# Kernel tuning notes

Hardware: AMD Instinct MI355X
Metric: run time of the kernel (lower is better)

The kernel has to match this reference:

```python
import jax, jax.numpy as jnp
import numpy as np

E = 192; Q = 48; H = 3; HD = Q // H  # per-branch embed 48, 3 heads of 16
CONV_CH = 4; K = 15; PAD = K // 2


def layer_norm(x, g, b, eps=1e-6):
    m = jnp.mean(x, axis=-1, keepdims=True)
    v = jnp.mean((x - m) ** 2, axis=-1, keepdims=True)
    return (x - m) * jax.lax.rsqrt(v + eps) * g + b


def mha(x, w_in, b_in, w_o, b_o):
    # x: [B,S,48]; torch nn.MultiheadAttention math (dropout=eval/identity)
    B, S, _ = x.shape
    qkv = x @ w_in.T + b_in                      # [B,S,144]
    q, k, v = jnp.split(qkv, 3, axis=-1)
    q = q.reshape(B, S, H, HD)
    k = k.reshape(B, S, H, HD)
    v = v.reshape(B, S, H, HD)
    scores = jnp.einsum('bqhd,bkhd->bhqk', q, k) / jnp.sqrt(jnp.float32(HD))
    attn = jax.nn.softmax(scores, axis=-1)
    out = jnp.einsum('bhqk,bkhd->bqhd', attn, v).reshape(B, S, Q)
    return out @ w_o.T + b_o


def light_conv(x96, conv_w):
    # x96: [B,S,96] -> view(-1, 4, 96), depthwise conv1d (k=15, pad=7), view back
    B, S, W = x96.shape
    r = x96.reshape(-1, CONV_CH, W)              # [B*S/... wait: B*S*96/(4*96)=B*S/4? No: reshape(-1,4,96) => [B*S, ...]
    y = jax.lax.conv_general_dilated(
        r, conv_w, window_strides=(1,), padding=[(PAD, PAD)],
        dimension_numbers=('NCH', 'OIH', 'NCH'), feature_group_count=CONV_CH)
    return y.reshape(B, S, W)


def setup_inputs() -> dict:
    key = jax.random.key(0)
    ks = jax.random.split(key, 16)
    sc = 0.05
    d = {
        'x': jax.random.normal(ks[0], (128, 512, E), dtype=jnp.float32),
        'ln1_g': jnp.ones((E,), jnp.float32), 'ln1_b': jnp.zeros((E,), jnp.float32),
        'acc_wqkv': jax.random.normal(ks[1], (3 * Q, Q), jnp.float32) * sc,
        'acc_bqkv': jnp.zeros((3 * Q,), jnp.float32),
        'acc_wo': jax.random.normal(ks[2], (Q, Q), jnp.float32) * sc,
        'acc_bo': jnp.zeros((Q,), jnp.float32),
        'gyro_wqkv': jax.random.normal(ks[3], (3 * Q, Q), jnp.float32) * sc,
        'gyro_bqkv': jnp.zeros((3 * Q,), jnp.float32),
        'gyro_wo': jax.random.normal(ks[4], (Q, Q), jnp.float32) * sc,
        'gyro_bo': jnp.zeros((Q,), jnp.float32),
        'conv_w': jax.random.normal(ks[5], (CONV_CH, 1, K), jnp.float32) * sc,
        'ln2_g': jnp.ones((E,), jnp.float32), 'ln2_b': jnp.zeros((E,), jnp.float32),
        'w1': jax.random.normal(ks[6], (2 * E, E), jnp.float32) * sc,
        'b1': jnp.zeros((2 * E,), jnp.float32),
        'w2': jax.random.normal(ks[7], (E, 2 * E), jnp.float32) * sc,
        'b2': jnp.zeros((E,), jnp.float32),
    }
    return d


def reference(x, ln1_g, ln1_b, acc_wqkv, acc_bqkv, acc_wo, acc_bo,
              gyro_wqkv, gyro_bqkv, gyro_wo, gyro_bo, conv_w,
              ln2_g, ln2_b, w1, b1, w2, b2):
    xn = layer_norm(x, ln1_g, ln1_b)
    x_conv = light_conv(xn[:, :, 48:144], conv_w)
    x_acc = mha(xn[:, :, 0:48], acc_wqkv, acc_bqkv, acc_wo, acc_bo)
    x_gyro = mha(xn[:, :, 96:144], gyro_wqkv, gyro_bqkv, gyro_wo, gyro_bo)
    xcat = jnp.concatenate([x_acc, x_conv, x_gyro], axis=2)
    x1 = xcat + x
    tt = layer_norm(x1, ln2_g, ln2_b)
    tt = jax.nn.relu(tt @ w1.T + b1)
    tt = jax.nn.relu(tt @ w2.T + b2)
    return x1 + tt
```

## Files before the change

### kernel.cpp

```cpp
#include <hip/hip_runtime.h>
#include <stdint.h>

typedef unsigned short u16;
typedef short bf16x8 __attribute__((ext_vector_type(8)));
typedef float f32x4 __attribute__((ext_vector_type(4)));
typedef float f32x16 __attribute__((ext_vector_type(16)));
typedef uint32_t u32x4 __attribute__((ext_vector_type(4)));

#define NB   128
#define SEQ  512
#define EMB  192
#define NTOK (NB * SEQ)
#define F1DIM 384
#define ATTW 192
#define VTP  520
#define KTS  24
#define XnS  200
#define H1S  392

__device__ __forceinline__ float bf2f(u16 u) {
  union { uint32_t u; float f; } v; v.u = ((uint32_t)u) << 16; return v.f;
}
__device__ __forceinline__ u16 f2bf(float f) {
  union { float f; uint32_t u; } v; v.f = f;
  uint32_t r = v.u + 0x7fffu + ((v.u >> 16) & 1u);
  return (u16)(r >> 16);
}
__device__ __forceinline__ uint32_t pack2bf(float a, float b) {
  return (uint32_t)f2bf(a) | ((uint32_t)f2bf(b) << 16);
}

__global__ __launch_bounds__(256) void pack_kernel(const float* __restrict__ w1,
    const float* __restrict__ w2, const float* __restrict__ wqa,
    const float* __restrict__ wqg, const float* __restrict__ woa,
    const float* __restrict__ wog, u16* __restrict__ w1b, u16* __restrict__ w2b,
    u16* __restrict__ wqp, u16* __restrict__ wop) {
  int idx = (int)blockIdx.x * 256 + (int)threadIdx.x;
  if (idx < 73728) {
    w1b[idx] = f2bf(w1[idx]);
  } else if (idx < 147456) {
    w2b[idx - 73728] = f2bf(w2[idx - 73728]);
  } else if (idx < 165888) {
    int i = idx - 147456;
    int row = i >> 6, k = i & 63;
    float v = 0.0f;
    if (k < 48) v = (row < 144) ? wqa[row * 48 + k] : wqg[(row - 144) * 48 + k];
    wqp[i] = f2bf(v);
  } else if (idx < 172032) {
    int i = idx - 165888;
    int row = i >> 6, k = i & 63;
    float v = 0.0f;
    if (k < 48) v = (row < 48) ? woa[row * 48 + k] : wog[(row - 48) * 48 + k];
    wop[i] = f2bf(v);
  }
}

__global__ __launch_bounds__(256) void ln1_qkv_conv_kernel(
    const float* __restrict__ x, const float* __restrict__ g,
    const float* __restrict__ b, const u16* __restrict__ wq,
    const float* __restrict__ bacc, const float* __restrict__ bgyr,
    const float* __restrict__ cw, u16* __restrict__ qkv,
    u16* __restrict__ att) {
  __shared__ u16 Xn[64 * XnS];
  int bm = (int)blockIdx.x * 64;
  int tid = threadIdx.x;
  int trow = tid >> 2, part = tid & 3;
  int tok = bm + trow;
  const float* xr = x + (size_t)tok * EMB + part * 48;
  float vals[48];
#pragma unroll
  for (int j = 0; j < 48; j += 4) {
    float4 v = *(const float4*)(xr + j);
    vals[j] = v.x; vals[j + 1] = v.y; vals[j + 2] = v.z; vals[j + 3] = v.w;
  }
  float s = 0.0f, s2 = 0.0f;
#pragma unroll
  for (int j = 0; j < 48; j++) { s += vals[j]; s2 += vals[j] * vals[j]; }
  s += __shfl_xor(s, 1); s2 += __shfl_xor(s2, 1);
  s += __shfl_xor(s, 2); s2 += __shfl_xor(s2, 2);
  float mean = s * (1.0f / EMB);
  float var  = s2 * (1.0f / EMB) - mean * mean;
  float rs   = rsqrtf(var + 1e-6f);
  {
    u16* xnrow = Xn + trow * XnS + part * 48;
    const float* gp = g + part * 48;
    const float* bp = b + part * 48;
#pragma unroll
    for (int j = 0; j < 48; j += 2) {
      uint32_t w = pack2bf((vals[j] - mean) * rs * gp[j] + bp[j],
                           (vals[j + 1] - mean) * rs * gp[j + 1] + bp[j + 1]);
      *(uint32_t*)(xnrow + j) = w;
    }
  }
  __syncthreads();
  int wid = tid >> 6, lane = tid & 63;
  int l15 = lane & 15, quad = lane >> 4;
  const u16* arow_l = Xn + (wid * 16 + l15) * XnS;
  f32x4 acc[18] = {};
#pragma unroll
  for (int ks = 0; ks < 2; ks++) {
    int kk = ks * 32;
    bf16x8 af_a = *(const bf16x8*)(arow_l + kk + quad * 8);
    bf16x8 af_g = *(const bf16x8*)(arow_l + 96 + kk + quad * 8);
#pragma unroll
    for (int st = 0; st < 18; st++) {
      bf16x8 bf = *(const bf16x8*)(wq + (size_t)(st * 16 + l15) * 64 + kk + quad * 8);
      acc[st] = __builtin_amdgcn_mfma_f32_16x16x32_bf16(st < 9 ? af_a : af_g,
                                                        bf, acc[st], 0, 0, 0);
    }
  }
#pragma unroll
  for (int st = 0; st < 18; st++) {
    int col = st * 16 + l15;
    int cc = (col < 144) ? col : col - 144;
    float bias = (col < 144) ? bacc[cc] : bgyr[cc];
    float qs = (cc < 48) ? 0.36067376022f : 1.0f;
#pragma unroll
    for (int r = 0; r < 4; r++) {
      int orow = bm + wid * 16 + quad * 4 + r;
      qkv[(size_t)orow * 288 + col] = f2bf((acc[st][r] + bias) * qs);
    }
  }
  {
    int wr = trow & 3;
    float w15[15];
#pragma unroll
    for (int k = 0; k < 15; k++) w15[k] = cw[wr * 15 + k];
    float win[38];
    int base = part * 24 - 7;
#pragma unroll
    for (int i = 0; i < 38; i++) {
      int p = base + i;
      win[i] = (p >= 0 && p < 96) ? bf2f(Xn[trow * XnS + 48 + p]) : 0.0f;
    }
    const float* xres = x + (size_t)tok * EMB + 48 + part * 24;
    u16* orow = att + (size_t)tok * ATTW + 96 + part * 24;
#pragma unroll
    for (int c = 0; c < 24; c += 4) {
      float4 r4 = *(const float4*)(xres + c);
      float o[4];
#pragma unroll
      for (int u = 0; u < 4; u++) {
        float sc = 0.0f;
#pragma unroll
        for (int k = 0; k < 15; k++) sc += win[c + u + k] * w15[k];
        o[u] = sc;
      }
      *(uint32_t*)(orow + c)     = pack2bf(o[0] + r4.x, o[1] + r4.y);
      *(uint32_t*)(orow + c + 2) = pack2bf(o[2] + r4.z, o[3] + r4.w);
    }
  }
}

__global__ __launch_bounds__(256) void attn_kernel(const u16* __restrict__ qkv,
                                                   u16* __restrict__ att) {
  __shared__ u16 Kt[SEQ * KTS];
  __shared__ u16 Vt[17 * VTP];
  int bid = blockIdx.x;
  int hh  = bid % 3;
  int brb = (bid / 3) & 1;
  int b   = bid / 6;
  int tid = threadIdx.x;
  size_t tokbase = (size_t)b * SEQ;
  int qoff = brb * 144 + hh * 16;
  int koff = qoff + 48;
  int voff = qoff + 96;
  for (int r = tid; r < SEQ; r += 256) {
    const u16* src = qkv + (tokbase + r) * 288;
    *(uint4*)(Kt + r * KTS)     = *(const uint4*)(src + koff);
    *(uint4*)(Kt + r * KTS + 8) = *(const uint4*)(src + koff + 8);
    u16 tmp[16];
    *(uint4*)(tmp)     = *(const uint4*)(src + voff);
    *(uint4*)(tmp + 8) = *(const uint4*)(src + voff + 8);
#pragma unroll
    for (int j = 0; j < 16; j++) Vt[j * VTP + r] = tmp[j];
  }
  Vt[16 * VTP + tid]       = 0x3F80;
  Vt[16 * VTP + 256 + tid] = 0x3F80;
  __syncthreads();
  int wave = tid >> 6, lane = tid & 63;
  int q31 = lane & 31, h = lane >> 5;
  int dcl = (q31 < 16) ? q31 : 16;
#pragma unroll 1
  for (int qi = 0; qi < 4; qi++) {
    int qrow = (wave * 4 + qi) * 32 + q31;
    bf16x8 qfrag = *(const bf16x8*)(qkv + (tokbase + qrow) * 288 + qoff + h * 8);
    f32x16 Ot = {};
#pragma unroll 2
    for (int kt = 0; kt < 16; kt++) {
      bf16x8 kfrag = *(const bf16x8*)(Kt + (kt * 32 + q31) * KTS + h * 8);
      f32x16 zc = {};
      f32x16 S = __builtin_amdgcn_mfma_f32_32x32x16_bf16(kfrag, qfrag, zc, 0, 0, 0);
      uint32_t pk[8], swk[8];
#pragma unroll
      for (int i = 0; i < 8; i++) {
        union { float f; uint32_t u; } a0, a1;
        a0.f = exp2f(S[2 * i]);
        a1.f = exp2f(S[2 * i + 1]);
        pk[i] = __builtin_amdgcn_perm(a1.u, a0.u, 0x07060302u);
        swk[i] = (uint32_t)__shfl_xor((int)pk[i], 32);
      }
      u32x4 t1 = { h ? swk[2] : pk[0], h ? swk[3] : pk[1],
                   h ? pk[2]  : swk[0], h ? pk[3]  : swk[1] };
      u32x4 t2 = { h ? swk[6] : pk[4], h ? swk[7] : pk[5],
                   h ? pk[6]  : swk[4], h ? pk[7]  : swk[5] };
      bf16x8 pb1 = __builtin_bit_cast(bf16x8, t1);
      bf16x8 pb2 = __builtin_bit_cast(bf16x8, t2);
      bf16x8 av1 = *(const bf16x8*)(Vt + dcl * VTP + kt * 32 + h * 8);
      bf16x8 av2 = *(const bf16x8*)(Vt + dcl * VTP + kt * 32 + 16 + h * 8);
      Ot = __builtin_amdgcn_mfma_f32_32x32x16_bf16(av1, pb1, Ot, 0, 0, 0);
      Ot = __builtin_amdgcn_mfma_f32_32x32x16_bf16(av2, pb2, Ot, 0, 0, 0);
    }
    float inv = 1.0f / Ot[8];
    u16* orow = att + (tokbase + qrow) * ATTW + brb * 48 + hh * 16 + 4 * h;
    uint2 st0 = { pack2bf(Ot[0] * inv, Ot[1] * inv),
                  pack2bf(Ot[2] * inv, Ot[3] * inv) };
    uint2 st1 = { pack2bf(Ot[4] * inv, Ot[5] * inv),
                  pack2bf(Ot[6] * inv, Ot[7] * inv) };
    *(uint2*)(orow)     = st0;
    *(uint2*)(orow + 8) = st1;
  }
}

__global__ __launch_bounds__(512) void tail_kernel(
    const u16* __restrict__ att, const u16* __restrict__ wo,
    const float* __restrict__ boacc, const float* __restrict__ bogyr,
    const float* __restrict__ x, const float* __restrict__ g2,
    const float* __restrict__ b2v, const u16* __restrict__ w1b,
    const float* __restrict__ b1, const u16* __restrict__ w2b,
    const float* __restrict__ b2, float* __restrict__ out) {
  __shared__ u16 LDSB[32 * XnS + 32 * H1S];
  u16* X1b = LDSB;
  u16* Tn  = LDSB + 32 * XnS;
  u16* H1  = LDSB + 32 * XnS;
  int bm = (int)blockIdx.x * 32;
  int tid = threadIdx.x;
  int wid = tid >> 6, lane = tid & 63;
  int l15 = lane & 15, quad = lane >> 4;

  if (wid >= 6) {
    int trow = (wid - 6) * 16 + (lane >> 2), p4 = lane & 3;
    const u16* src = att + (size_t)(bm + trow) * ATTW + 96 + p4 * 24;
    u16* dst = X1b + trow * XnS + 48 + p4 * 24;
    *(uint4*)(dst)      = *(const uint4*)(src);
    *(uint4*)(dst + 8)  = *(const uint4*)(src + 8);
    *(uint4*)(dst + 16) = *(const uint4*)(src + 16);
  } else {
    int st = wid;
    int ng = (st >= 3) ? 1 : 0;
    f32x4 acc[2] = {};
    bf16x8 wf[2];
#pragma unroll
    for (int ks = 0; ks < 2; ks++)
      wf[ks] = *(const bf16x8*)(wo + (size_t)(st * 16 + l15) * 64 + ks * 32 + quad * 8);
#pragma unroll
    for (int m = 0; m < 2; m++) {
      const u16* arow = att + (size_t)(bm + m * 16 + l15) * ATTW + (ng ? 48 : 0);
#pragma unroll
      for (int ks = 0; ks < 2; ks++) {
        bf16x8 af = *(const bf16x8*)(arow + ks * 32 + quad * 8);
        acc[m] = __builtin_amdgcn_mfma_f32_16x16x32_bf16(af, wf[ks], acc[m], 0, 0, 0);
      }
    }
    int col = st * 16 + l15;
    float bias = (col < 48) ? boacc[col] : bogyr[col - 48];
    int oc = (col < 48) ? col : col + 96;
#pragma unroll
    for (int m = 0; m < 2; m++) {
#pragma unroll
      for (int r = 0; r < 4; r++) {
        int lrow = m * 16 + quad * 4 + r;
        float v = acc[m][r] + bias + x[(size_t)(bm + lrow) * EMB + oc];
        X1b[lrow * XnS + oc] = f2bf(v);
      }
    }
  }
  __syncthreads();

  {
    int trow = tid >> 4, part = tid & 15;
    const u16* xl = X1b + trow * XnS + part * 12;
    u16 raw[12];
    *(uint2*)(raw)     = *(const uint2*)(xl);
    *(uint2*)(raw + 4) = *(const uint2*)(xl + 4);
    *(uint2*)(raw + 8) = *(const uint2*)(xl + 8);
    float vals[12];
#pragma unroll
    for (int j = 0; j < 12; j++) vals[j] = bf2f(raw[j]);
    float s = 0.0f, s2 = 0.0f;
#pragma unroll
    for (int j = 0; j < 12; j++) { s += vals[j]; s2 += vals[j] * vals[j]; }
    s += __shfl_xor(s, 1); s2 += __shfl_xor(s2, 1);
    s += __shfl_xor(s, 2); s2 += __shfl_xor(s2, 2);
    s += __shfl_xor(s, 4); s2 += __shfl_xor(s2, 4);
    s += __shfl_xor(s, 8); s2 += __shfl_xor(s2, 8);
    float mean = s * (1.0f / EMB);
    float var  = s2 * (1.0f / EMB) - mean * mean;
    float rs   = rsqrtf(var + 1e-6f);
    u16* trp = Tn + trow * XnS + part * 12;
    const float* gp = g2 + part * 12;
    const float* bp = b2v + part * 12;
#pragma unroll
    for (int j = 0; j < 12; j += 2) {
      uint32_t w = pack2bf((vals[j] - mean) * rs * gp[j] + bp[j],
                           (vals[j + 1] - mean) * rs * gp[j + 1] + bp[j + 1]);
      *(uint32_t*)(trp + j) = w;
    }
  }
  __syncthreads();

  int mg = wid & 1, ng = wid >> 1;
  f32x4 acc1[6] = {};
#pragma unroll
  for (int kk = 0; kk < 192; kk += 32) {
    bf16x8 a0 = *(const bf16x8*)(Tn + (mg * 16 + l15) * XnS + kk + quad * 8);
#pragma unroll
    for (int stl = 0; stl < 6; stl++) {
      bf16x8 bf = *(const bf16x8*)(w1b + (size_t)((ng * 6 + stl) * 16 + l15) * EMB + kk + quad * 8);
      acc1[stl] = __builtin_amdgcn_mfma_f32_16x16x32_bf16(a0, bf, acc1[stl], 0, 0, 0);
    }
  }
  __syncthreads();
#pragma unroll
  for (int stl = 0; stl < 6; stl++) {
    int col = (ng * 6 + stl) * 16 + l15;
    float bias = b1[col];
#pragma unroll
    for (int r = 0; r < 4; r++) {
      float v = acc1[stl][r] + bias;
      v = v > 0.0f ? v : 0.0f;
      H1[(mg * 16 + quad * 4 + r) * H1S + col] = f2bf(v);
    }
  }
  __syncthreads();

  {
    f32x4 acc2[3] = {};
#pragma unroll
    for (int kk = 0; kk < 384; kk += 32) {
      bf16x8 a0 = *(const bf16x8*)(H1 + (mg * 16 + l15) * H1S + kk + quad * 8);
#pragma unroll
      for (int stl = 0; stl < 3; stl++) {
        bf16x8 bf = *(const bf16x8*)(w2b + (size_t)((ng * 3 + stl) * 16 + l15) * F1DIM + kk + quad * 8);
        acc2[stl] = __builtin_amdgcn_mfma_f32_16x16x32_bf16(a0, bf, acc2[stl], 0, 0, 0);
      }
    }
#pragma unroll
    for (int stl = 0; stl < 3; stl++) {
      int col = (ng * 3 + stl) * 16 + l15;
      float bias = b2[col];
#pragma unroll
      for (int r = 0; r < 4; r++) {
        int lrow = mg * 16 + quad * 4 + r;
        float v = acc2[stl][r] + bias;
        v = v > 0.0f ? v : 0.0f;
        out[(size_t)(bm + lrow) * EMB + col] = v + bf2f(X1b[lrow * XnS + col]);
      }
    }
  }
}

extern "C" void kernel_launch(void* const* d_in, const int* in_sizes, int n_in,
                              void* d_out, int out_size, void* d_ws, size_t ws_size,
                              hipStream_t stream) {
  const float* x         = (const float*)d_in[0];
  const float* ln1_g     = (const float*)d_in[1];
  const float* ln1_b     = (const float*)d_in[2];
  const float* acc_wqkv  = (const float*)d_in[3];
  const float* acc_bqkv  = (const float*)d_in[4];
  const float* acc_wo    = (const float*)d_in[5];
  const float* acc_bo    = (const float*)d_in[6];
  const float* gyro_wqkv = (const float*)d_in[7];
  const float* gyro_bqkv = (const float*)d_in[8];
  const float* gyro_wo   = (const float*)d_in[9];
  const float* gyro_bo   = (const float*)d_in[10];
  const float* conv_w    = (const float*)d_in[11];
  const float* ln2_g     = (const float*)d_in[12];
  const float* ln2_b     = (const float*)d_in[13];
  const float* w1        = (const float*)d_in[14];
  const float* b1        = (const float*)d_in[15];
  const float* w2        = (const float*)d_in[16];
  const float* b2        = (const float*)d_in[17];
  float* out = (float*)d_out;
  char* ws = (char*)d_ws;

  u16* qkvb = (u16*)(ws);
  u16* attb = (u16*)(ws + 37748736);
  u16* w1b  = (u16*)(ws + 62914560);
  u16* w2b  = (u16*)(ws + 63062016);
  u16* wqp  = (u16*)(ws + 63209472);
  u16* wop  = (u16*)(ws + 63246336);

  pack_kernel<<<672, 256, 0, stream>>>(w1, w2, acc_wqkv, gyro_wqkv, acc_wo,
                                       gyro_wo, w1b, w2b, wqp, wop);
  ln1_qkv_conv_kernel<<<NTOK / 64, 256, 0, stream>>>(
      x, ln1_g, ln1_b, wqp, acc_bqkv, gyro_bqkv, conv_w, qkvb, attb);
  attn_kernel<<<NB * 6, 256, 0, stream>>>(qkvb, attb);
  tail_kernel<<<NTOK / 32, 512, 0, stream>>>(
      attb, wop, acc_bo, gyro_bo, x, ln2_g, ln2_b, w1b, b1, w2b, b2, out);
}
```

Before: 369.6 us.

## Split fused tail into out-proj+LN2, FFN1, FFN2 kernels with LDS-resident weights

Replaces the single fused tail kernel with three kernels. The first does the out-projection, residual and LN2, writing normalized activations to global memory. The other two are persistent-style FFN kernels that stage w1/w2 into LDS once per block and loop over 256 tokens, so each block stops re-reading the weights from global/L2. The cost is round-trips through HBM for the normalized activations (192 bf16 per token) and the FFN hidden layer (384 bf16 per token), plus extra launches. The residual x1 is stored back into the attention buffer and reused in ffn2 through a remapped column offset.

```diff
diff --git a/kernel.cpp b/kernel.cpp
--- a/kernel.cpp
+++ b/kernel.cpp
@@ -16,7 +16,10 @@
 #define VTP  520
 #define KTS  24
 #define XnS  200
-#define H1S  392
+#define TNW  192
+#define H1W  384
+#define W1S  200
+#define W2S  392
 
 __device__ __forceinline__ float bf2f(u16 u) {
   union { uint32_t u; float f; } v; v.u = ((uint32_t)u) << 16; return v.f;
@@ -222,139 +225,200 @@
   }
 }
 
-__global__ __launch_bounds__(512) void tail_kernel(
-    const u16* __restrict__ att, const u16* __restrict__ wo,
+__global__ __launch_bounds__(256) void outproj_ln2_kernel(
+    u16* __restrict__ att, const u16* __restrict__ wo,
     const float* __restrict__ boacc, const float* __restrict__ bogyr,
     const float* __restrict__ x, const float* __restrict__ g2,
-    const float* __restrict__ b2v, const u16* __restrict__ w1b,
-    const float* __restrict__ b1, const u16* __restrict__ w2b,
-    const float* __restrict__ b2, float* __restrict__ out) {
-  __shared__ u16 LDSB[32 * XnS + 32 * H1S];
-  u16* X1b = LDSB;
-  u16* Tn  = LDSB + 32 * XnS;
-  u16* H1  = LDSB + 32 * XnS;
-  int bm = (int)blockIdx.x * 32;
+    const float* __restrict__ b2v, u16* __restrict__ tn) {
+  __shared__ u16 X1[64 * XnS];
+  int bm = (int)blockIdx.x * 64;
   int tid = threadIdx.x;
   int wid = tid >> 6, lane = tid & 63;
   int l15 = lane & 15, quad = lane >> 4;
-
-  if (wid >= 6) {
-    int trow = (wid - 6) * 16 + (lane >> 2), p4 = lane & 3;
-    const u16* src = att + (size_t)(bm + trow) * ATTW + 96 + p4 * 24;
-    u16* dst = X1b + trow * XnS + 48 + p4 * 24;
-    *(uint4*)(dst)      = *(const uint4*)(src);
-    *(uint4*)(dst + 8)  = *(const uint4*)(src + 8);
-    *(uint4*)(dst + 16) = *(const uint4*)(src + 16);
+  if (wid < 2) {
+    bf16x8 wf[2][3];
+#pragma unroll
+    for (int s = 0; s < 3; s++) {
+      int st = wid * 3 + s;
+#pragma unroll
+      for (int ks = 0; ks < 2; ks++)
+        wf[ks][s] = *(const bf16x8*)(wo + (size_t)(st * 16 + l15) * 64 + ks * 32 + quad * 8);
+    }
+    f32x4 acc[4][3] = {};
+#pragma unroll
+    for (int m = 0; m < 4; m++) {
+      const u16* ar = att + (size_t)(bm + m * 16 + l15) * ATTW + (wid ? 48 : 0);
+#pragma unroll
+      for (int ks = 0; ks < 2; ks++) {
+        bf16x8 af = *(const bf16x8*)(ar + ks * 32 + quad * 8);
+#pragma unroll
+        for (int s = 0; s < 3; s++)
+          acc[m][s] = __builtin_amdgcn_mfma_f32_16x16x32_bf16(af, wf[ks][s], acc[m][s], 0, 0, 0);
+      }
+    }
+#pragma unroll
+    for (int s = 0; s < 3; s++) {
+      int col = (wid * 3 + s) * 16 + l15;
+      float bias = (col < 48) ? boacc[col] : bogyr[col - 48];
+      int oc = (col < 48) ? col : col + 96;
+#pragma unroll
+      for (int m = 0; m < 4; m++) {
+#pragma unroll
+        for (int r = 0; r < 4; r++) {
+          int lrow = m * 16 + quad * 4 + r;
+          float v = acc[m][s][r] + bias + x[(size_t)(bm + lrow) * EMB + oc];
+          u16 bv = f2bf(v);
+          X1[lrow * XnS + oc] = bv;
+          att[(size_t)(bm + lrow) * ATTW + col] = bv;
+        }
+      }
+    }
   } else {
-    int st = wid;
-    int ng = (st >= 3) ? 1 : 0;
-    f32x4 acc[2] = {};
-    bf16x8 wf[2];
-#pragma unroll
-    for (int ks = 0; ks < 2; ks++)
-      wf[ks] = *(const bf16x8*)(wo + (size_t)(st * 16 + l15) * 64 + ks * 32 + quad * 8);
-#pragma unroll
-    for (int m = 0; m < 2; m++) {
-      const u16* arow = att + (size_t)(bm + m * 16 + l15) * ATTW + (ng ? 48 : 0);
-#pragma unroll
-      for (int ks = 0; ks < 2; ks++) {
-        bf16x8 af = *(const bf16x8*)(arow + ks * 32 + quad * 8);
-        acc[m] = __builtin_amdgcn_mfma_f32_16x16x32_bf16(af, wf[ks], acc[m], 0, 0, 0);
-      }
-    }
-    int col = st * 16 + l15;
-    float bias = (col < 48) ? boacc[col] : bogyr[col - 48];
-    int oc = (col < 48) ? col : col + 96;
-#pragma unroll
-    for (int m = 0; m < 2; m++) {
-#pragma unroll
-      for (int r = 0; r < 4; r++) {
-        int lrow = m * 16 + quad * 4 + r;
-        float v = acc[m][r] + bias + x[(size_t)(bm + lrow) * EMB + oc];
-        X1b[lrow * XnS + oc] = f2bf(v);
-      }
-    }
+    int trow = (wid - 2) * 32 + (lane >> 1);
+    int half = lane & 1;
+    const u16* src = att + (size_t)(bm + trow) * ATTW + 96 + half * 48;
+    u16* dst = X1 + trow * XnS + 48 + half * 48;
+#pragma unroll
+    for (int j = 0; j < 48; j += 8)
+      *(uint4*)(dst + j) = *(const uint4*)(src + j);
   }
   __syncthreads();
-
   {
-    int trow = tid >> 4, part = tid & 15;
-    const u16* xl = X1b + trow * XnS + part * 12;
-    u16 raw[12];
-    *(uint2*)(raw)     = *(const uint2*)(xl);
-    *(uint2*)(raw + 4) = *(const uint2*)(xl + 4);
-    *(uint2*)(raw + 8) = *(const uint2*)(xl + 8);
-    float vals[12];
-#pragma unroll
-    for (int j = 0; j < 12; j++) vals[j] = bf2f(raw[j]);
+    int trow = tid >> 2, part = tid & 3;
+    const u16* xl = X1 + trow * XnS + part * 48;
+    float vals[48];
+#pragma unroll
+    for (int j = 0; j < 48; j += 8) {
+      u16 raw[8];
+      *(uint4*)raw = *(const uint4*)(xl + j);
+#pragma unroll
+      for (int u = 0; u < 8; u++) vals[j + u] = bf2f(raw[u]);
+    }
     float s = 0.0f, s2 = 0.0f;
 #pragma unroll
-    for (int j = 0; j < 12; j++) { s += vals[j]; s2 += vals[j] * vals[j]; }
+    for (int j = 0; j < 48; j++) { s += vals[j]; s2 += vals[j] * vals[j]; }
     s += __shfl_xor(s, 1); s2 += __shfl_xor(s2, 1);
     s += __shfl_xor(s, 2); s2 += __shfl_xor(s2, 2);
-    s += __shfl_xor(s, 4); s2 += __shfl_xor(s2, 4);
-    s += __shfl_xor(s, 8); s2 += __shfl_xor(s2, 8);
     float mean = s * (1.0f / EMB);
     float var  = s2 * (1.0f / EMB) - mean * mean;
     float rs   = rsqrtf(var + 1e-6f);
-    u16* trp = Tn + trow * XnS + part * 12;
-    const float* gp = g2 + part * 12;
-    const float* bp = b2v + part * 12;
-#pragma unroll
-    for (int j = 0; j < 12; j += 2) {
+    const float* gp = g2 + part * 48;
+    const float* bp = b2v + part * 48;
+    u16 obuf[48];
+#pragma unroll
+    for (int j = 0; j < 48; j += 2) {
       uint32_t w = pack2bf((vals[j] - mean) * rs * gp[j] + bp[j],
                            (vals[j + 1] - mean) * rs * gp[j + 1] + bp[j + 1]);
-      *(uint32_t*)(trp + j) = w;
-    }
+      *(uint32_t*)(obuf + j) = w;
+    }
+    u16* tr = tn + (size_t)(bm + trow) * TNW + part * 48;
+#pragma unroll
+    for (int j = 0; j < 48; j += 8)
+      *(uint4*)(tr + j) = *(const uint4*)(obuf + j);
+  }
+}
+
+__global__ __launch_bounds__(512) void ffn1_kernel(const u16* __restrict__ tn,
+    const u16* __restrict__ w1b, const float* __restrict__ b1,
+    u16* __restrict__ h1) {
+  __shared__ u16 W1[384 * W1S];
+  int tid = threadIdx.x;
+  for (int i = tid; i < 384 * 24; i += 512) {
+    int r = i / 24, sg = i % 24;
+    *(uint4*)(W1 + r * W1S + sg * 8) = *(const uint4*)(w1b + r * 192 + sg * 8);
   }
   __syncthreads();
-
-  int mg = wid & 1, ng = wid >> 1;
-  f32x4 acc1[6] = {};
-#pragma unroll
-  for (int kk = 0; kk < 192; kk += 32) {
-    bf16x8 a0 = *(const bf16x8*)(Tn + (mg * 16 + l15) * XnS + kk + quad * 8);
-#pragma unroll
-    for (int stl = 0; stl < 6; stl++) {
-      bf16x8 bf = *(const bf16x8*)(w1b + (size_t)((ng * 6 + stl) * 16 + l15) * EMB + kk + quad * 8);
-      acc1[stl] = __builtin_amdgcn_mfma_f32_16x16x32_bf16(a0, bf, acc1[stl], 0, 0, 0);
-    }
+  int wid = tid >> 6, lane = tid & 63;
+  int l15 = lane & 15, quad = lane >> 4;
+  int tok0 = (int)blockIdx.x * 256;
+  float bias[3];
+#pragma unroll
+  for (int s = 0; s < 3; s++) bias[s] = b1[(wid * 3 + s) * 16 + l15];
+#pragma unroll 1
+  for (int mc = 0; mc < 4; mc++) {
+    int tb = tok0 + mc * 64;
+    f32x4 acc[4][3] = {};
+#pragma unroll
+    for (int kk = 0; kk < 192; kk += 32) {
+      bf16x8 af[4];
+#pragma unroll
+      for (int m = 0; m < 4; m++)
+        af[m] = *(const bf16x8*)(tn + (size_t)(tb + m * 16 + l15) * TNW + kk + quad * 8);
+#pragma unroll
+      for (int s = 0; s < 3; s++) {
+        bf16x8 bf = *(const bf16x8*)(W1 + (size_t)((wid * 3 + s) * 16 + l15) * W1S + kk + quad * 8);
+#pragma unroll
+        for (int m = 0; m < 4; m++)
+          acc[m][s] = __builtin_amdgcn_mfma_f32_16x16x32_bf16(af[m], bf, acc[m][s], 0, 0, 0);
+      }
+    }
+#pragma unroll
+    for (int m = 0; m < 4; m++) {
+#pragma unroll
+      for (int s = 0; s < 3; s++) {
+        int col = (wid * 3 + s) * 16 + l15;
+#pragma unroll
+        for (int r = 0; r < 4; r++) {
+          float v = acc[m][s][r] + bias[s];
+          v = v > 0.0f ? v : 0.0f;
+          h1[(size_t)(tb + m * 16 + quad * 4 + r) * H1W + col] = f2bf(v);
+        }
+      }
+    }
+  }
+}
+
+__global__ __launch_bounds__(384) void ffn2_kernel(const u16* __restrict__ h1,
+    const u16* __restrict__ w2b, const float* __restrict__ b2,
+    const u16* __restrict__ att, float* __restrict__ out) {
+  __shared__ u16 W2[192 * W2S];
+  int tid = threadIdx.x;
+  for (int i = tid; i < 192 * 48; i += 384) {
+    int r = i / 48, sg = i % 48;
+    *(uint4*)(W2 + r * W2S + sg * 8) = *(const uint4*)(w2b + r * 384 + sg * 8);
   }
   __syncthreads();
-#pragma unroll
-  for (int stl = 0; stl < 6; stl++) {
-    int col = (ng * 6 + stl) * 16 + l15;
-    float bias = b1[col];
-#pragma unroll
-    for (int r = 0; r < 4; r++) {
-      float v = acc1[stl][r] + bias;
-      v = v > 0.0f ? v : 0.0f;
-      H1[(mg * 16 + quad * 4 + r) * H1S + col] = f2bf(v);
-    }
-  }
-  __syncthreads();
-
-  {
-    f32x4 acc2[3] = {};
+  int wid = tid >> 6, lane = tid & 63;
+  int l15 = lane & 15, quad = lane >> 4;
+  int tok0 = (int)blockIdx.x * 256;
+  float bias[2];
+  int aoff[2];
+#pragma unroll
+  for (int s = 0; s < 2; s++) {
+    int col = (wid * 2 + s) * 16 + l15;
+    bias[s] = b2[col];
+    aoff[s] = (col < 48) ? col : ((col < 144) ? col + 48 : col - 96);
+  }
+#pragma unroll 1
+  for (int mc = 0; mc < 4; mc++) {
+    int tb = tok0 + mc * 64;
+    f32x4 acc[4][2] = {};
 #pragma unroll
     for (int kk = 0; kk < 384; kk += 32) {
-      bf16x8 a0 = *(const bf16x8*)(H1 + (mg * 16 + l15) * H1S + kk + quad * 8);
-#pragma unroll
-      for (int stl = 0; stl < 3; stl++) {
-        bf16x8 bf = *(const bf16x8*)(w2b + (size_t)((ng * 3 + stl) * 16 + l15) * F1DIM + kk + quad * 8);
-        acc2[stl] = __builtin_amdgcn_mfma_f32_16x16x32_bf16(a0, bf, acc2[stl], 0, 0, 0);
-      }
-    }
-#pragma unroll
-    for (int stl = 0; stl < 3; stl++) {
-      int col = (ng * 3 + stl) * 16 + l15;
-      float bias = b2[col];
-#pragma unroll
-      for (int r = 0; r < 4; r++) {
-        int lrow = mg * 16 + quad * 4 + r;
-        float v = acc2[stl][r] + bias;
-        v = v > 0.0f ? v : 0.0f;
-        out[(size_t)(bm + lrow) * EMB + col] = v + bf2f(X1b[lrow * XnS + col]);
+      bf16x8 af[4];
+#pragma unroll
+      for (int m = 0; m < 4; m++)
+        af[m] = *(const bf16x8*)(h1 + (size_t)(tb + m * 16 + l15) * H1W + kk + quad * 8);
+#pragma unroll
+      for (int s = 0; s < 2; s++) {
+        bf16x8 bf = *(const bf16x8*)(W2 + (size_t)((wid * 2 + s) * 16 + l15) * W2S + kk + quad * 8);
+#pragma unroll
+        for (int m = 0; m < 4; m++)
+          acc[m][s] = __builtin_amdgcn_mfma_f32_16x16x32_bf16(af[m], bf, acc[m][s], 0, 0, 0);
+      }
+    }
+#pragma unroll
+    for (int m = 0; m < 4; m++) {
+#pragma unroll
+      for (int s = 0; s < 2; s++) {
+        int col = (wid * 2 + s) * 16 + l15;
+#pragma unroll
+        for (int r = 0; r < 4; r++) {
+          int tok = tb + m * 16 + quad * 4 + r;
+          float v = acc[m][s][r] + bias[s];
+          v = v > 0.0f ? v : 0.0f;
+          out[(size_t)tok * EMB + col] = v + bf2f(att[(size_t)tok * ATTW + aoff[s]]);
+        }
       }
     }
   }
@@ -385,17 +449,21 @@
   char* ws = (char*)d_ws;
 
   u16* qkvb = (u16*)(ws);
+  u16* tnb  = (u16*)(ws);
   u16* attb = (u16*)(ws + 37748736);
   u16* w1b  = (u16*)(ws + 62914560);
   u16* w2b  = (u16*)(ws + 63062016);
   u16* wqp  = (u16*)(ws + 63209472);
   u16* wop  = (u16*)(ws + 63246336);
+  u16* h1b  = (u16*)(ws + 63258624);
 
   pack_kernel<<<672, 256, 0, stream>>>(w1, w2, acc_wqkv, gyro_wqkv, acc_wo,
                                        gyro_wo, w1b, w2b, wqp, wop);
   ln1_qkv_conv_kernel<<<NTOK / 64, 256, 0, stream>>>(
       x, ln1_g, ln1_b, wqp, acc_bqkv, gyro_bqkv, conv_w, qkvb, attb);
   attn_kernel<<<NB * 6, 256, 0, stream>>>(qkvb, attb);
-  tail_kernel<<<NTOK / 32, 512, 0, stream>>>(
-      attb, wop, acc_bo, gyro_bo, x, ln2_g, ln2_b, w1b, b1, w2b, b2, out);
-}
+  outproj_ln2_kernel<<<NTOK / 64, 256, 0, stream>>>(
+      attb, wop, acc_bo, gyro_bo, x, ln2_g, ln2_b, tnb);
+  ffn1_kernel<<<256, 512, 0, stream>>>(tnb, w1b, b1, h1b);
+  ffn2_kernel<<<256, 384, 0, stream>>>(h1b, w2b, b2, attb, out);
+}
```

Result: faster. 336.9 us (-8.9%).
